# Kernel tuning notes

Measured on AMD Instinct MI355X. Metric: run time of the kernel, lower is better.

Reference implementation:

```python
import jax, jax.numpy as jnp
import numpy as np

N = 65536
K = 4096          # codebook_size
D = 512           # d_model

def setup_inputs() -> dict:
    key = jax.random.key(0)
    k1, k2 = jax.random.split(key)
    z = jax.random.normal(k1, (N, D), dtype=jnp.float32)
    weight = jax.random.normal(k2, (K, D), dtype=jnp.float32)
    return {"z": z, "weight": weight}

def reference(z, weight):
    # squared L2 distances: ||z||^2 + ||w||^2 - 2 z @ w^T  -> [N, K]
    z_sq = jnp.sum(z * z, axis=1, keepdims=True)            # [N, 1]
    w_sq = jnp.sum(weight * weight, axis=1)                 # [K]
    distances = z_sq + w_sq - 2.0 * jnp.matmul(z, weight.T) # [N, K]
    indices = jnp.argmin(distances, axis=1)                 # [N] int
    quantized = jnp.take(weight, indices, axis=0)           # [N, D]
    return indices, quantized
```

## Files before the change

kernel.cpp:

```cpp
#include <hip/hip_runtime.h>

#define N_ROWS  65536
#define K_CB    4096
#define D_MODEL 512
#define TAU     0.35f
#define CAPA    8192
#define CAPB    8192

typedef __attribute__((ext_vector_type(8))) _Float16 f16x8;
typedef __attribute__((ext_vector_type(4))) float f32x4;
typedef unsigned int        u32;
typedef unsigned long long  u64;

__device__ __forceinline__ void load_lds16(const void* g, void* l) {
    __builtin_amdgcn_global_load_lds(
        (const __attribute__((address_space(1))) u32*)g,
        (__attribute__((address_space(3))) u32*)l, 16, 0, 0);
}

__device__ __forceinline__ u32 ordf(float f) {
    u32 u = __float_as_uint(f);
    return (u >> 31) ? ~u : (u | 0x80000000u);
}

__global__ __launch_bounds__(256) void convert_z(const float* __restrict__ z,
                                                 _Float16* __restrict__ zh) {
    size_t i = ((size_t)blockIdx.x * 256 + threadIdx.x) * 8;
    float4 a = *(const float4*)(z + i);
    float4 b = *(const float4*)(z + i + 4);
    f16x8 o;
    o[0] = (_Float16)a.x; o[1] = (_Float16)a.y; o[2] = (_Float16)a.z; o[3] = (_Float16)a.w;
    o[4] = (_Float16)b.x; o[5] = (_Float16)b.y; o[6] = (_Float16)b.z; o[7] = (_Float16)b.w;
    *(f16x8*)(zh + i) = o;
}

__global__ __launch_bounds__(256) void convert_w(const float* __restrict__ w,
                                                 _Float16* __restrict__ wh,
                                                 float* __restrict__ wsq,
                                                 int* __restrict__ counterA,
                                                 int* __restrict__ counterB) {
    if (blockIdx.x == 0 && threadIdx.x == 0) { *counterA = 0; *counterB = 0; }
    int k    = blockIdx.x * 4 + (threadIdx.x >> 6);
    int lane = threadIdx.x & 63;
    const float4* row = (const float4*)(w + (size_t)k * D_MODEL);
    float s = 0.f;
    #pragma unroll
    for (int c = 0; c < 2; ++c) {
        float4 v = row[lane + 64 * c];
        s += v.x * v.x + v.y * v.y + v.z * v.z + v.w * v.w;
        _Float16* o = wh + (size_t)k * D_MODEL + (lane + 64 * c) * 4;
        o[0] = (_Float16)v.x; o[1] = (_Float16)v.y; o[2] = (_Float16)v.z; o[3] = (_Float16)v.w;
    }
    #pragma unroll
    for (int m = 32; m; m >>= 1) s += __shfl_xor(s, m, 64);
    if (lane == 0) wsq[k] = s;
}

__global__ __launch_bounds__(256, 2) void gemm_argmin(
    const _Float16* __restrict__ zh, const _Float16* __restrict__ wh,
    const float* __restrict__ w, const float* __restrict__ wsq,
    float* __restrict__ out_idx, float* __restrict__ out_q,
    int4* __restrict__ listA, int* __restrict__ listB, u64* __restrict__ slots,
    int* __restrict__ counterA, int* __restrict__ counterB) {
    __shared__ _Float16 As[2][128 * 64];
    __shared__ _Float16 Bs[2][128 * 64];
    __shared__ int idx_s[128];

    const int tid  = threadIdx.x;
    const int lane = tid & 63;
    const int wv   = tid >> 6;
    const int m0   = blockIdx.x * 128;
    const int l15  = lane & 15;
    const int g    = lane >> 4;

    const int srow = lane >> 3;
    const int scol = (lane & 7) ^ srow;

    float v1[8], v2[8], v3[8]; int i1[8], i2[8];
    #pragma unroll
    for (int i = 0; i < 8; ++i) { v1[i] = 3.4e38f; v2[i] = 3.4e38f; v3[i] = 3.4e38f; i1[i] = 0; i2[i] = 0; }

    auto STAGE = [&](int kts, int d0s, int b) {
        const int ch = wv << 2;
        const _Float16* as = zh + (size_t)(m0 + (ch << 3) + srow) * D_MODEL + d0s + scol * 8;
        #pragma unroll
        for (int q = 0; q < 4; ++q)
            load_lds16(as + (size_t)(q * 8) * D_MODEL, &As[b][(ch + q) << 9]);
        const _Float16* bs = wh + (size_t)(kts * 128 + (ch << 3) + srow) * D_MODEL + d0s + scol * 8;
        #pragma unroll
        for (int q = 0; q < 4; ++q)
            load_lds16(bs + (size_t)(q * 8) * D_MODEL, &Bs[b][(ch + q) << 9]);
    };

    STAGE(0, 0, 0);

    for (int kt = 0; kt < 32; ++kt) {
        f32x4 acc[2][8];
        float wq[8];
        #pragma unroll
        for (int dc = 0; dc < 8; ++dc) {
            const int cur = dc & 1;
            if (dc < 7) {
                STAGE(kt, (dc + 1) << 6, cur ^ 1);
                asm volatile("s_waitcnt vmcnt(8)" ::: "memory");
            } else if (kt < 31) {
                STAGE(kt + 1, 0, cur ^ 1);
                asm volatile("s_waitcnt vmcnt(8)" ::: "memory");
            } else {
                asm volatile("s_waitcnt vmcnt(0)" ::: "memory");
            }
            __builtin_amdgcn_s_barrier();
            __builtin_amdgcn_sched_barrier(0);

            if (dc == 0) {
                #pragma unroll
                for (int n = 0; n < 8; ++n) {
                    acc[0][n] = (f32x4){0.f, 0.f, 0.f, 0.f};
                    acc[1][n] = (f32x4){0.f, 0.f, 0.f, 0.f};
                    wq[n] = wsq[(kt << 7) + (n << 4) + l15];
                }
            }

            __builtin_amdgcn_s_setprio(1);
            #pragma unroll
            for (int h = 0; h < 2; ++h) {
                const int colq = (h << 2) + g;
                f16x8 af[2];
                #pragma unroll
                for (int m = 0; m < 2; ++m) {
                    const int r = (wv << 5) + (m << 4) + l15;
                    af[m] = *(const f16x8*)&As[cur][(r << 6) + ((colq ^ (r & 7)) << 3)];
                }
                #pragma unroll
                for (int n = 0; n < 8; ++n) {
                    const int br = (n << 4) + l15;
                    f16x8 bv = *(const f16x8*)&Bs[cur][(br << 6) + ((colq ^ (br & 7)) << 3)];
                    #pragma unroll
                    for (int m = 0; m < 2; ++m)
                        acc[m][n] = __builtin_amdgcn_mfma_f32_16x16x32_f16(af[m], bv, acc[m][n], 0, 0, 0);
                }
            }
            __builtin_amdgcn_s_setprio(0);

            if (dc == 7) {
                #pragma unroll
                for (int n = 0; n < 8; ++n) {
                    int k = (kt << 7) + (n << 4) + l15;
                    #pragma unroll
                    for (int m = 0; m < 2; ++m)
                        #pragma unroll
                        for (int r = 0; r < 4; ++r) {
                            float s = fmaf(-2.f, acc[m][n][r], wq[n]);
                            int rs = (m << 2) + r;
                            if (s < v3[rs]) {
                                if (s < v1[rs]) {
                                    v3[rs] = v2[rs]; v2[rs] = v1[rs]; i2[rs] = i1[rs];
                                    v1[rs] = s; i1[rs] = k;
                                } else if (s < v2[rs]) {
                                    v3[rs] = v2[rs]; v2[rs] = s; i2[rs] = k;
                                } else v3[rs] = s;
                            }
                        }
                }
            }
            __builtin_amdgcn_sched_barrier(0);
            __builtin_amdgcn_s_barrier();
        }
    }

    #pragma unroll
    for (int rs = 0; rs < 8; ++rs) {
        float a1 = v1[rs], a2 = v2[rs], a3 = v3[rs];
        int   j1 = i1[rs], j2 = i2[rs];
        #pragma unroll
        for (int off = 1; off < 16; off <<= 1) {
            float b1 = __shfl_xor(a1, off);
            float b2 = __shfl_xor(a2, off);
            float b3 = __shfl_xor(a3, off);
            int   k1 = __shfl_xor(j1, off);
            int   k2 = __shfl_xor(j2, off);
            bool l1 = (b1 < a1) || (b1 == a1 && k1 < j1);
            bool l2 = (b1 < a2) || (b1 == a2 && k1 < j2);
            bool l3 = (b1 < a3);
            if (l1)      { a3 = a2; a2 = a1; j2 = j1; a1 = b1; j1 = k1; }
            else if (l2) { a3 = a2; a2 = b1; j2 = k1; }
            else if (l3) { a3 = b1; }
            bool m2 = (b2 < a2) || (b2 == a2 && k2 < j2);
            bool m3 = (b2 < a3);
            if (m2)      { a3 = a2; a2 = b2; j2 = k2; }
            else if (m3) { a3 = b2; }
            a3 = fminf(a3, b3);
        }
        if (l15 == 0) {
            int rl = (wv << 5) + ((rs >> 2) << 4) + (g << 2) + (rs & 3);
            int row = m0 + rl;
            out_idx[row] = (float)j1;
            idx_s[rl] = j1;
            float lim = a1 + TAU;
            if (a3 <= lim) {
                int p = atomicAdd(counterB, 1);
                if (p < CAPB) { listB[p] = row; slots[p] = ~0ull; }
            } else if (a2 <= lim) {
                int p = atomicAdd(counterA, 1);
                if (p < CAPA) listA[p] = make_int4(row, j1, j2, 0);
                else {
                    int q = atomicAdd(counterB, 1);
                    if (q < CAPB) { listB[q] = row; slots[q] = ~0ull; }
                }
            }
        }
    }
    __syncthreads();

    const float4* w4 = (const float4*)w;
    float4* o4 = (float4*)out_q;
    for (int c = tid; c < 128 * 128; c += 256) {
        int r = c >> 7, cc = c & 127;
        o4[(size_t)(m0 + r) * 128 + cc] = w4[(size_t)idx_s[r] * 128 + cc];
    }
}

__global__ __launch_bounds__(256) void verify_pairs(
    const float* __restrict__ z, const float* __restrict__ w,
    const float* __restrict__ wsq, const int4* __restrict__ listA,
    const int* __restrict__ counterA,
    float* __restrict__ out_idx, float* __restrict__ out_q) {
    int cA = *counterA; if (cA > CAPA) cA = CAPA;
    for (int e = blockIdx.x * 256 + threadIdx.x; e < cA; e += gridDim.x * 256) {
        int4 ent = listA[e];
        const float4* zr = (const float4*)(z + (size_t)ent.x * D_MODEL);
        const float4* wa = (const float4*)(w + (size_t)ent.y * D_MODEL);
        const float4* wb = (const float4*)(w + (size_t)ent.z * D_MODEL);
        float d1 = 0.f, d2 = 0.f;
        #pragma unroll 8
        for (int c = 0; c < 128; ++c) {
            float4 zv = zr[c];
            float4 a  = wa[c];
            float4 b  = wb[c];
            d1 = fmaf(zv.x, a.x, d1); d1 = fmaf(zv.y, a.y, d1);
            d1 = fmaf(zv.z, a.z, d1); d1 = fmaf(zv.w, a.w, d1);
            d2 = fmaf(zv.x, b.x, d2); d2 = fmaf(zv.y, b.y, d2);
            d2 = fmaf(zv.z, b.z, d2); d2 = fmaf(zv.w, b.w, d2);
        }
        float s1 = fmaf(-2.f, d1, wsq[ent.y]);
        float s2 = fmaf(-2.f, d2, wsq[ent.z]);
        int win = (s2 < s1 || (s2 == s1 && ent.z < ent.y)) ? ent.z : ent.y;
        if (win != ent.y) {
            out_idx[ent.x] = (float)win;
            const float4* src = (const float4*)(w + (size_t)win * D_MODEL);
            float4* dst = (float4*)(out_q + (size_t)ent.x * D_MODEL);
            for (int c = 0; c < 128; ++c) dst[c] = src[c];
        }
    }
}

__global__ __launch_bounds__(256) void fullscan_part(
    const float* __restrict__ z, const float* __restrict__ w,
    const float* __restrict__ wsq, const int* __restrict__ listB,
    const int* __restrict__ counterB, u64* __restrict__ slots) {
    __shared__ float zs[D_MODEL];
    __shared__ u64 red[4];
    int cB = *counterB; if (cB > CAPB) cB = CAPB;
    int items = cB * 4;
    const int lane = threadIdx.x & 63;
    const int wv   = threadIdx.x >> 6;
    for (int it = blockIdx.x; it < items; it += gridDim.x) {
        int p = it >> 2, q = it & 3;
        int row = listB[p];
        __syncthreads();
        for (int c = threadIdx.x; c < D_MODEL; c += 256) zs[c] = z[(size_t)row * D_MODEL + c];
        __syncthreads();
        int kb = q * 1024 + threadIdx.x * 4;
        const float* wr = w + (size_t)kb * D_MODEL;
        float acc[4] = {0.f, 0.f, 0.f, 0.f};
        for (int c = 0; c < 128; ++c) {
            float4 zv = ((const float4*)zs)[c];
            #pragma unroll
            for (int r = 0; r < 4; ++r) {
                float4 wvv = ((const float4*)(wr + (size_t)r * D_MODEL))[c];
                acc[r] = fmaf(zv.x, wvv.x, acc[r]); acc[r] = fmaf(zv.y, wvv.y, acc[r]);
                acc[r] = fmaf(zv.z, wvv.z, acc[r]); acc[r] = fmaf(zv.w, wvv.w, acc[r]);
            }
        }
        float bv = 3.4e38f; int bi = 0;
        #pragma unroll
        for (int r = 0; r < 4; ++r) {
            float s = fmaf(-2.f, acc[r], wsq[kb + r]);
            if (s < bv) { bv = s; bi = kb + r; }
        }
        u64 key = ((u64)ordf(bv) << 32) | (u32)bi;
        #pragma unroll
        for (int off = 32; off; off >>= 1) {
            u64 o = __shfl_xor(key, off);
            if (o < key) key = o;
        }
        if (lane == 0) red[wv] = key;
        __syncthreads();
        if (threadIdx.x == 0) {
            u64 m = red[0];
            if (red[1] < m) m = red[1];
            if (red[2] < m) m = red[2];
            if (red[3] < m) m = red[3];
            atomicMin(&slots[p], m);
        }
    }
}

__global__ __launch_bounds__(256) void fullscan_final(
    const float* __restrict__ w, const int* __restrict__ listB,
    const int* __restrict__ counterB, const u64* __restrict__ slots,
    float* __restrict__ out_idx, float* __restrict__ out_q) {
    int cB = *counterB; if (cB > CAPB) cB = CAPB;
    const int wv = threadIdx.x >> 6, lane = threadIdx.x & 63;
    for (int p = blockIdx.x * 4 + wv; p < cB; p += gridDim.x * 4) {
        int row = listB[p];
        int win = (int)(u32)(slots[p] & 0xFFFFFFFFull);
        if (lane == 0) out_idx[row] = (float)win;
        const float4* src = (const float4*)(w + (size_t)win * D_MODEL);
        float4* dst = (float4*)(out_q + (size_t)row * D_MODEL);
        dst[lane] = src[lane];
        dst[lane + 64] = src[lane + 64];
    }
}

__global__ __launch_bounds__(256) void wsq_kernel(const float* __restrict__ w,
                                                  float* __restrict__ wsq) {
    int k    = blockIdx.x * 4 + (threadIdx.x >> 6);
    int lane = threadIdx.x & 63;
    const float4* row = (const float4*)(w + (size_t)k * D_MODEL);
    float s = 0.f;
    #pragma unroll
    for (int c = 0; c < 2; ++c) {
        float4 v = row[lane + 64 * c];
        s += v.x * v.x + v.y * v.y + v.z * v.z + v.w * v.w;
    }
    #pragma unroll
    for (int m = 32; m; m >>= 1) s += __shfl_xor(s, m, 64);
    if (lane == 0) wsq[k] = s;
}

__global__ __launch_bounds__(256) void vq_fp32(const float* __restrict__ z,
                                               const float* __restrict__ w,
                                               const float* __restrict__ wsq,
                                               float* __restrict__ out_idx,
                                               float* __restrict__ out_q) {
    __shared__ float zs[64][36];
    __shared__ float ws[128][36];
    __shared__ int   idx_s[64];
    const int tid = threadIdx.x;
    const int tx  = tid & 15;
    const int ty  = tid >> 4;
    const int m0  = blockIdx.x * 64;
    float minv[4]; int mini[4];
    #pragma unroll
    for (int i = 0; i < 4; ++i) { minv[i] = 3.4e38f; mini[i] = 0; }
    for (int k0 = 0; k0 < K_CB; k0 += 128) {
        float acc[4][8];
        #pragma unroll
        for (int i = 0; i < 4; ++i)
            #pragma unroll
            for (int j = 0; j < 8; ++j) acc[i][j] = 0.f;
        for (int d0 = 0; d0 < D_MODEL; d0 += 32) {
            __syncthreads();
            {
                int r = tid >> 3, c = tid & 7;
                #pragma unroll
                for (int it = 0; it < 2; ++it, r += 32)
                    *(float4*)&zs[r][c * 4] = ((const float4*)(z + (size_t)(m0 + r) * D_MODEL + d0))[c];
            }
            {
                int r = tid >> 3, c = tid & 7;
                #pragma unroll
                for (int it = 0; it < 4; ++it, r += 32)
                    *(float4*)&ws[r][c * 4] = ((const float4*)(w + (size_t)(k0 + r) * D_MODEL + d0))[c];
            }
            __syncthreads();
            #pragma unroll
            for (int d = 0; d < 32; d += 4) {
                float4 zv[4];
                #pragma unroll
                for (int i = 0; i < 4; ++i) zv[i] = *(const float4*)&zs[ty * 4 + i][d];
                float4 wv[8];
                #pragma unroll
                for (int j = 0; j < 8; ++j) wv[j] = *(const float4*)&ws[j * 16 + tx][d];
                #pragma unroll
                for (int i = 0; i < 4; ++i)
                    #pragma unroll
                    for (int j = 0; j < 8; ++j) {
                        acc[i][j] = fmaf(zv[i].x, wv[j].x, acc[i][j]);
                        acc[i][j] = fmaf(zv[i].y, wv[j].y, acc[i][j]);
                        acc[i][j] = fmaf(zv[i].z, wv[j].z, acc[i][j]);
                        acc[i][j] = fmaf(zv[i].w, wv[j].w, acc[i][j]);
                    }
            }
        }
        #pragma unroll
        for (int j = 0; j < 8; ++j) {
            int   k  = k0 + j * 16 + tx;
            float wq = wsq[k];
            #pragma unroll
            for (int i = 0; i < 4; ++i) {
                float s = fmaf(-2.f, acc[i][j], wq);
                if (s < minv[i]) { minv[i] = s; mini[i] = k; }
            }
        }
    }
    #pragma unroll
    for (int i = 0; i < 4; ++i) {
        float v = minv[i]; int ix = mini[i];
        #pragma unroll
        for (int m = 8; m; m >>= 1) {
            float ov = __shfl_xor(v, m, 16);
            int   oi = __shfl_xor(ix, m, 16);
            if (ov < v || (ov == v && oi < ix)) { v = ov; ix = oi; }
        }
        if (tx == 0) {
            int row = ty * 4 + i;
            out_idx[m0 + row] = (float)ix;
            idx_s[row] = ix;
        }
    }
    __syncthreads();
    const float4* w4 = (const float4*)w;
    float4*       o4 = (float4*)out_q;
    for (int t = tid; t < 64 * 128; t += 256) {
        int r = t >> 7, c = t & 127;
        o4[(size_t)(m0 + r) * 128 + c] = w4[(size_t)idx_s[r] * 128 + c];
    }
}

extern "C" void kernel_launch(void* const* d_in, const int* in_sizes, int n_in,
                              void* d_out, int out_size, void* d_ws, size_t ws_size,
                              hipStream_t stream) {
    const float* z = (const float*)d_in[0];
    const float* w = (const float*)d_in[1];
    float* out_idx = (float*)d_out;
    float* out_q   = (float*)d_out + N_ROWS;

    const size_t off_listA = 256;
    const size_t off_listB = off_listA + (size_t)CAPA * 16;
    const size_t off_slots = off_listB + (size_t)CAPB * 4;
    const size_t off_wsq   = off_slots + (size_t)CAPB * 8;
    const size_t off_wh    = off_wsq + (size_t)K_CB * 4;
    const size_t off_zh    = off_wh + (size_t)K_CB * D_MODEL * 2;
    const size_t NEED      = off_zh + (size_t)N_ROWS * D_MODEL * 2;

    if (ws_size >= NEED) {
        char* ws = (char*)d_ws;
        int*  counterA = (int*)ws;
        int*  counterB = (int*)(ws + 4);
        int4* listA    = (int4*)(ws + off_listA);
        int*  listB    = (int*)(ws + off_listB);
        u64*  slots    = (u64*)(ws + off_slots);
        float* wsq     = (float*)(ws + off_wsq);
        _Float16* wh   = (_Float16*)(ws + off_wh);
        _Float16* zh   = (_Float16*)(ws + off_zh);

        convert_z<<<(N_ROWS * D_MODEL) / (256 * 8), 256, 0, stream>>>(z, zh);
        convert_w<<<K_CB / 4, 256, 0, stream>>>(w, wh, wsq, counterA, counterB);
        gemm_argmin<<<N_ROWS / 128, 256, 0, stream>>>(zh, wh, w, wsq, out_idx, out_q,
                                                      listA, listB, slots,
                                                      counterA, counterB);
        verify_pairs<<<64, 256, 0, stream>>>(z, w, wsq, listA, counterA, out_idx, out_q);
        fullscan_part<<<512, 256, 0, stream>>>(z, w, wsq, listB, counterB, slots);
        fullscan_final<<<64, 256, 0, stream>>>(w, listB, counterB, slots, out_idx, out_q);
    } else {
        float* wsq = (float*)d_ws;
        wsq_kernel<<<K_CB / 4, 256, 0, stream>>>(w, wsq);
        vq_fp32<<<N_ROWS / 64, 256, 0, stream>>>(z, w, wsq, out_idx, out_q);
    }
}
```

Baseline: 880.7 us.

## Shrink GEMM tile to 64 rows with 2x2 wave split and LDS top-3 merge

Each block now covers 64 z rows instead of 128, and its four waves form a 2x2 grid where each wave handles 32 rows by 64 codebook columns. This halves the A tile in LDS and the accumulator registers, which allows three blocks per CU and doubles the grid size. Because two waves now share each row, their per-row top-3 candidates are merged through LDS before the list and atomic logic runs. The setprio hints are removed. The cost is that each block reuses every codebook tile across fewer rows, so codebook traffic from L2 doubles and LDS reads per MFMA go up.

Measured after the change: 868.9 us. About the same (-1.3%).

```diff
diff --git a/kernel.cpp b/kernel.cpp
--- a/kernel.cpp
+++ b/kernel.cpp
@@ -56,20 +56,22 @@
     if (lane == 0) wsq[k] = s;
 }
 
-__global__ __launch_bounds__(256, 2) void gemm_argmin(
+__global__ __launch_bounds__(256, 3) void gemm_argmin(
     const _Float16* __restrict__ zh, const _Float16* __restrict__ wh,
     const float* __restrict__ w, const float* __restrict__ wsq,
     float* __restrict__ out_idx, float* __restrict__ out_q,
     int4* __restrict__ listA, int* __restrict__ listB, u64* __restrict__ slots,
     int* __restrict__ counterA, int* __restrict__ counterB) {
-    __shared__ _Float16 As[2][128 * 64];
+    __shared__ _Float16 As[2][64 * 64];
     __shared__ _Float16 Bs[2][128 * 64];
-    __shared__ int idx_s[128];
+    __shared__ int idx_s[64];
 
     const int tid  = threadIdx.x;
     const int lane = tid & 63;
     const int wv   = tid >> 6;
-    const int m0   = blockIdx.x * 128;
+    const int wr   = wv >> 1;
+    const int wc   = wv & 1;
+    const int m0   = blockIdx.x * 64;
     const int l15  = lane & 15;
     const int g    = lane >> 4;
 
@@ -81,31 +83,31 @@
     for (int i = 0; i < 8; ++i) { v1[i] = 3.4e38f; v2[i] = 3.4e38f; v3[i] = 3.4e38f; i1[i] = 0; i2[i] = 0; }
 
     auto STAGE = [&](int kts, int d0s, int b) {
-        const int ch = wv << 2;
-        const _Float16* as = zh + (size_t)(m0 + (ch << 3) + srow) * D_MODEL + d0s + scol * 8;
+        const int chA = wv << 1;
+        const _Float16* as = zh + (size_t)(m0 + (chA << 3) + srow) * D_MODEL + d0s + scol * 8;
+        load_lds16(as,                       &As[b][chA << 9]);
+        load_lds16(as + (size_t)8 * D_MODEL, &As[b][(chA + 1) << 9]);
+        const int chB = wv << 2;
+        const _Float16* bs = wh + (size_t)(kts * 128 + (chB << 3) + srow) * D_MODEL + d0s + scol * 8;
         #pragma unroll
         for (int q = 0; q < 4; ++q)
-            load_lds16(as + (size_t)(q * 8) * D_MODEL, &As[b][(ch + q) << 9]);
-        const _Float16* bs = wh + (size_t)(kts * 128 + (ch << 3) + srow) * D_MODEL + d0s + scol * 8;
-        #pragma unroll
-        for (int q = 0; q < 4; ++q)
-            load_lds16(bs + (size_t)(q * 8) * D_MODEL, &Bs[b][(ch + q) << 9]);
+            load_lds16(bs + (size_t)(q * 8) * D_MODEL, &Bs[b][(chB + q) << 9]);
     };
 
     STAGE(0, 0, 0);
 
     for (int kt = 0; kt < 32; ++kt) {
-        f32x4 acc[2][8];
-        float wq[8];
+        f32x4 acc[2][4];
+        float wq[4];
         #pragma unroll
         for (int dc = 0; dc < 8; ++dc) {
             const int cur = dc & 1;
             if (dc < 7) {
                 STAGE(kt, (dc + 1) << 6, cur ^ 1);
-                asm volatile("s_waitcnt vmcnt(8)" ::: "memory");
+                asm volatile("s_waitcnt vmcnt(6)" ::: "memory");
             } else if (kt < 31) {
                 STAGE(kt + 1, 0, cur ^ 1);
-                asm volatile("s_waitcnt vmcnt(8)" ::: "memory");
+                asm volatile("s_waitcnt vmcnt(6)" ::: "memory");
             } else {
                 asm volatile("s_waitcnt vmcnt(0)" ::: "memory");
             }
@@ -114,38 +116,36 @@
 
             if (dc == 0) {
                 #pragma unroll
-                for (int n = 0; n < 8; ++n) {
+                for (int n = 0; n < 4; ++n) {
                     acc[0][n] = (f32x4){0.f, 0.f, 0.f, 0.f};
                     acc[1][n] = (f32x4){0.f, 0.f, 0.f, 0.f};
-                    wq[n] = wsq[(kt << 7) + (n << 4) + l15];
+                    wq[n] = wsq[(kt << 7) + (wc << 6) + (n << 4) + l15];
                 }
             }
 
-            __builtin_amdgcn_s_setprio(1);
             #pragma unroll
             for (int h = 0; h < 2; ++h) {
                 const int colq = (h << 2) + g;
                 f16x8 af[2];
                 #pragma unroll
                 for (int m = 0; m < 2; ++m) {
-                    const int r = (wv << 5) + (m << 4) + l15;
+                    const int r = (wr << 5) + (m << 4) + l15;
                     af[m] = *(const f16x8*)&As[cur][(r << 6) + ((colq ^ (r & 7)) << 3)];
                 }
                 #pragma unroll
-                for (int n = 0; n < 8; ++n) {
-                    const int br = (n << 4) + l15;
+                for (int n = 0; n < 4; ++n) {
+                    const int br = (wc << 6) + (n << 4) + l15;
                     f16x8 bv = *(const f16x8*)&Bs[cur][(br << 6) + ((colq ^ (br & 7)) << 3)];
                     #pragma unroll
                     for (int m = 0; m < 2; ++m)
                         acc[m][n] = __builtin_amdgcn_mfma_f32_16x16x32_f16(af[m], bv, acc[m][n], 0, 0, 0);
                 }
             }
-            __builtin_amdgcn_s_setprio(0);
 
             if (dc == 7) {
                 #pragma unroll
-                for (int n = 0; n < 8; ++n) {
-                    int k = (kt << 7) + (n << 4) + l15;
+                for (int n = 0; n < 4; ++n) {
+                    int k = (kt << 7) + (wc << 6) + (n << 4) + l15;
                     #pragma unroll
                     for (int m = 0; m < 2; ++m)
                         #pragma unroll
@@ -168,6 +168,9 @@
         }
     }
 
+    __syncthreads();
+    float* hv = (float*)&Bs[0][0];
+    int*   hi = (int*)&Bs[0][0];
     #pragma unroll
     for (int rs = 0; rs < 8; ++rs) {
         float a1 = v1[rs], a2 = v2[rs], a3 = v3[rs];
@@ -192,21 +195,48 @@
             a3 = fminf(a3, b3);
         }
         if (l15 == 0) {
-            int rl = (wv << 5) + ((rs >> 2) << 4) + (g << 2) + (rs & 3);
-            int row = m0 + rl;
-            out_idx[row] = (float)j1;
-            idx_s[rl] = j1;
-            float lim = a1 + TAU;
-            if (a3 <= lim) {
-                int p = atomicAdd(counterB, 1);
-                if (p < CAPB) { listB[p] = row; slots[p] = ~0ull; }
-            } else if (a2 <= lim) {
-                int p = atomicAdd(counterA, 1);
-                if (p < CAPA) listA[p] = make_int4(row, j1, j2, 0);
-                else {
-                    int q = atomicAdd(counterB, 1);
-                    if (q < CAPB) { listB[q] = row; slots[q] = ~0ull; }
-                }
+            int rowb = (wr << 5) + ((rs >> 2) << 4) + (g << 2) + (rs & 3);
+            int base = (wc << 6) | rowb;
+            hv[base]       = a1;
+            hv[128 + base] = a2;
+            hv[256 + base] = a3;
+            hi[384 + base] = j1;
+            hi[512 + base] = j2;
+        }
+    }
+    __syncthreads();
+
+    if (tid < 64) {
+        int row = tid;
+        float a1 = hv[row],       a2 = hv[128 + row], a3 = hv[256 + row];
+        int   j1 = hi[384 + row], j2 = hi[512 + row];
+        float b1 = hv[64 + row],  b2 = hv[192 + row], b3 = hv[320 + row];
+        int   k1 = hi[448 + row], k2 = hi[576 + row];
+        bool l1 = (b1 < a1) || (b1 == a1 && k1 < j1);
+        bool l2 = (b1 < a2) || (b1 == a2 && k1 < j2);
+        bool l3 = (b1 < a3);
+        if (l1)      { a3 = a2; a2 = a1; j2 = j1; a1 = b1; j1 = k1; }
+        else if (l2) { a3 = a2; a2 = b1; j2 = k1; }
+        else if (l3) { a3 = b1; }
+        bool m2 = (b2 < a2) || (b2 == a2 && k2 < j2);
+        bool m3 = (b2 < a3);
+        if (m2)      { a3 = a2; a2 = b2; j2 = k2; }
+        else if (m3) { a3 = b2; }
+        a3 = fminf(a3, b3);
+
+        int grow = m0 + row;
+        out_idx[grow] = (float)j1;
+        idx_s[row] = j1;
+        float lim = a1 + TAU;
+        if (a3 <= lim) {
+            int p = atomicAdd(counterB, 1);
+            if (p < CAPB) { listB[p] = grow; slots[p] = ~0ull; }
+        } else if (a2 <= lim) {
+            int p = atomicAdd(counterA, 1);
+            if (p < CAPA) listA[p] = make_int4(grow, j1, j2, 0);
+            else {
+                int q = atomicAdd(counterB, 1);
+                if (q < CAPB) { listB[q] = grow; slots[q] = ~0ull; }
             }
         }
     }
@@ -214,7 +244,7 @@
 
     const float4* w4 = (const float4*)w;
     float4* o4 = (float4*)out_q;
-    for (int c = tid; c < 128 * 128; c += 256) {
+    for (int c = tid; c < 64 * 128; c += 256) {
         int r = c >> 7, cc = c & 127;
         o4[(size_t)(m0 + r) * 128 + cc] = w4[(size_t)idx_s[r] * 128 + cc];
     }
@@ -458,9 +488,9 @@
 
         convert_z<<<(N_ROWS * D_MODEL) / (256 * 8), 256, 0, stream>>>(z, zh);
         convert_w<<<K_CB / 4, 256, 0, stream>>>(w, wh, wsq, counterA, counterB);
-        gemm_argmin<<<N_ROWS / 128, 256, 0, stream>>>(zh, wh, w, wsq, out_idx, out_q,
-                                                      listA, listB, slots,
-                                                      counterA, counterB);
+        gemm_argmin<<<N_ROWS / 64, 256, 0, stream>>>(zh, wh, w, wsq, out_idx, out_q,
+                                                     listA, listB, slots,
+                                                     counterA, counterB);
         verify_pairs<<<64, 256, 0, stream>>>(z, w, wsq, listA, counterA, out_idx, out_q);
         fullscan_part<<<512, 256, 0, stream>>>(z, w, wsq, listB, counterB, slots);
         fullscan_final<<<64, 256, 0, stream>>>(w, listB, counterB, slots, out_idx, out_q);
```
